# Optimization experiments

Measured on AMD Instinct MI355X. Metric: run time of the kernel, lower is better.

The kernel has to match this reference:

```python
import jax, jax.numpy as jnp
import numpy as np

LAMBDA_TV = 0.01
RHO = 1.0
MAX_ITER = 10
CG_ITER = 10


def _fft2c(x):
    # x: (B, 2, H, W) real/imag stacked -> centered ortho FFT, same layout
    xc = x[:, 0] + 1j * x[:, 1]
    kc = jnp.fft.fftshift(
        jnp.fft.fft2(jnp.fft.ifftshift(xc, axes=(-2, -1)), norm='ortho'),
        axes=(-2, -1))
    return jnp.stack([kc.real, kc.imag], axis=1)


def _ifft2c(x):
    xc = x[:, 0] + 1j * x[:, 1]
    ic = jnp.fft.fftshift(
        jnp.fft.ifft2(jnp.fft.ifftshift(xc, axes=(-2, -1)), norm='ortho'),
        axes=(-2, -1))
    return jnp.stack([ic.real, ic.imag], axis=1)


def _gradient(x):
    # forward differences, zero at the far boundary; cat along channel dim
    dx = jnp.concatenate([x[..., 1:] - x[..., :-1], jnp.zeros_like(x[..., :1])], axis=-1)
    dy = jnp.concatenate([x[..., 1:, :] - x[..., :-1, :], jnp.zeros_like(x[..., :1, :])], axis=-2)
    return jnp.concatenate([dx, dy], axis=1)


def _divergence(p):
    # Faithful to the original: only uses channels 0 and 1 of p -> (B,1,H,W)
    px, py = p[:, 0:1], p[:, 1:2]
    div_x = jnp.concatenate(
        [px[..., 0:1], px[..., 1:-1] - px[..., :-2], -px[..., -2:-1]], axis=-1)
    div_y = jnp.concatenate(
        [py[..., 0:1, :], py[..., 1:-1, :] - py[..., :-2, :], -py[..., -2:-1, :]], axis=-2)
    return div_x + div_y


def soft_threshold(x, t):
    return jnp.sign(x) * jnp.maximum(jnp.abs(x) - t, 0.0)


def _cg_solve(x0, b, mask):
    # Solves (F^H M F + rho * D^H D) x = b with early-stop semantics of the original
    def A(z):
        return _ifft2c(mask * _fft2c(z)) - RHO * _divergence(_gradient(z))

    r0 = b - A(x0)
    rsold0 = jnp.sum(r0 * r0)

    def step(carry, _):
        x, r, p, rsold, done = carry
        Ap = A(p)
        alpha = rsold / (jnp.sum(p * Ap) + 1e-12)
        xn = x + alpha * p
        rn = r - alpha * Ap
        rsnew = jnp.sum(rn * rn)
        stop = rsnew < 1e-10
        pn = rn + (rsnew / rsold) * p
        x = jnp.where(done, x, xn)
        r = jnp.where(done, r, rn)
        p = jnp.where(done | stop, p, pn)
        rsold = jnp.where(done | stop, rsold, rsnew)
        done = done | stop
        return (x, r, p, rsold, done), None

    init = (x0, r0, r0, rsold0, jnp.array(False))
    (x, _, _, _, _), _ = jax.lax.scan(step, init, None, length=CG_ITER)
    return x


def reference(y, mask):
    x0 = _ifft2c(y)
    u0 = _gradient(x0)
    v0 = jnp.zeros_like(u0)
    b_data = _ifft2c(mask * y)  # constant across outer iterations
    thresh = LAMBDA_TV / RHO

    def step(carry, _):
        x, u, v, done, count, pres_l, dres_l = carry
        b = b_data + RHO * _divergence(u - v)
        xn = _cg_solve(x, b, mask)
        g = _gradient(xn)
        un = soft_threshold(g + v, thresh)
        vn = v + g - un
        pres = jnp.linalg.norm(g - un)
        dres = jnp.linalg.norm(RHO * _divergence(un - u))
        stop = (pres < 1e-4) & (dres < 1e-4)
        x = jnp.where(done, x, xn)
        u = jnp.where(done, u, un)
        v = jnp.where(done, v, vn)
        pres_l = jnp.where(done, pres_l, pres)
        dres_l = jnp.where(done, dres_l, dres)
        count = count + (1 - done.astype(jnp.int32))
        done = done | stop
        return (x, u, v, done, count, pres_l, dres_l), None

    init = (x0, u0, v0, jnp.array(False), jnp.array(0, jnp.int32),
            jnp.array(0.0, x0.dtype), jnp.array(0.0, x0.dtype))
    (x, _, _, _, count, pres, dres), _ = jax.lax.scan(step, init, None, length=MAX_ITER)
    return x, count, pres, dres


def setup_inputs() -> dict:
    key = jax.random.key(0)
    k1, k2 = jax.random.split(key)
    B, H, W = 4, 320, 320
    y = jax.random.normal(k1, (B, 2, H, W), dtype=jnp.float32)
    mask = (jax.random.uniform(k2, (B, 1, H, W)) < 0.3).astype(jnp.float32)
    return {"y": y, "mask": mask}
```

## Files before the change

### kernel.cpp

```cpp
#include <hip/hip_runtime.h>
#include <math.h>

#define DEVFN __device__ __forceinline__

namespace {

constexpr int NW = 320, NH = 320, NHW = NW * NH, NB = 4;
constexpr int NC2 = 2 * NHW;
constexpr int GRID = NB * NH;
constexpr int NTHR = 320;
constexpr float THRESHc = 0.01f;

struct C2 { float x, y; };
DEVFN C2 cmul(C2 a, C2 b) { return C2{a.x * b.x - a.y * b.y, a.x * b.y + a.y * b.x}; }

template <int SIGN>
DEVFN C2 TW(const float2* tw, int m) {
  float2 t = tw[m];
  return C2{t.x, (SIGN < 0) ? t.y : -t.y};
}

DEVFN int swzcol(int bid) { return (bid & 7) * (GRID / 8) + (bid >> 3); }

DEVFN int oidx(int t) { return 5 * (t & 63) + (t >> 6); }

DEVFN void wavebar() {
  __builtin_amdgcn_wave_barrier();
  asm volatile("" ::: "memory");
}

template <int SIGN, bool MASKED>
__device__ C2 fftp_core(const float2* IN, float2* SCR, const float2* tw, int t,
                        const float* __restrict__ misRow) {
  const int q = t >> 6, n1 = t & 63;
  float2* lo = SCR + q * 128;
  float2* hi = lo + 64;
  float mval = 1.f;
  if (MASKED) mval = misRow[5 * n1 + q];
  C2 acc;
  {
    float2 v0 = IN[n1];
    acc.x = v0.x; acc.y = v0.y;
#pragma unroll
    for (int n2 = 1; n2 < 5; n2++) {
      float2 v = IN[n1 + 64 * n2];
      C2 w = TW<SIGN>(tw, 64 * ((n2 * q) % 5));
      acc.x += v.x * w.x - v.y * w.y;
      acc.y += v.x * w.y + v.y * w.x;
    }
    acc = cmul(acc, TW<SIGN>(tw, n1 * q));
  }
  lo[n1] = make_float2(acc.x, acc.y);
  wavebar();
  {
    C2 s{0.f, 0.f};
    int rr = n1 & 3, base = n1 >> 2;
#pragma unroll
    for (int p = 0; p < 4; p++) {
      float2 v = lo[base + 16 * p];
      C2 w = TW<SIGN>(tw, 80 * ((p * rr) & 3));
      s.x += v.x * w.x - v.y * w.y;
      s.y += v.x * w.y + v.y * w.x;
    }
    hi[n1] = make_float2(s.x, s.y);
  }
  wavebar();
  {
    C2 s{0.f, 0.f};
    int rr = n1 & 15, base = ((n1 >> 4) << 2) + (n1 & 3);
#pragma unroll
    for (int p = 0; p < 4; p++) {
      float2 v = hi[base + 16 * p];
      C2 w = TW<SIGN>(tw, 20 * ((p * rr) & 15));
      s.x += v.x * w.x - v.y * w.y;
      s.y += v.x * w.y + v.y * w.x;
    }
    lo[n1] = make_float2(s.x, s.y);
  }
  wavebar();
  {
    C2 s{0.f, 0.f};
    int base = n1 & 15;
#pragma unroll
    for (int p = 0; p < 4; p++) {
      float2 v = lo[base + 16 * p];
      C2 w = TW<SIGN>(tw, 5 * ((p * n1) & 63));
      s.x += v.x * w.x - v.y * w.y;
      s.y += v.x * w.y + v.y * w.x;
    }
    acc = s;
  }
  if (MASKED) { acc.x *= mval; acc.y *= mval; }
  return acc;
}

DEVFN float Gfunc2(const float2* __restrict__ z, int b, int h, int w) {
  const float2* zz = z + b * NHW;
  int hw = h * NW + w;
  float divx, divy;
  if (w == 0) {
    divx = zz[hw + 1].x - zz[hw].x;
  } else if (w < NW - 1) {
    divx = (zz[hw + 1].x - zz[hw].x) - (zz[hw].x - zz[hw - 1].x);
  } else {
    divx = -(zz[hw].x - zz[hw - 1].x);
  }
  if (h == 0) {
    divy = (w < NW - 1) ? zz[hw + 1].y - zz[hw].y : 0.f;
  } else if (h < NH - 1) {
    float a = (w < NW - 1) ? zz[hw + 1].y - zz[hw].y : 0.f;
    float bb = (w < NW - 1) ? zz[hw - NW + 1].y - zz[hw - NW].y : 0.f;
    divy = a - bb;
  } else {
    divy = -((w < NW - 1) ? zz[hw - NW + 1].y - zz[hw - NW].y : 0.f);
  }
  return divx + divy;
}

DEVFN float divUV(const float* __restrict__ u, const float* __restrict__ v, int b, int h, int w) {
  const float* u0 = u + (b * 4 + 0) * NHW; const float* v0 = v + (b * 4 + 0) * NHW;
  const float* u1 = u + (b * 4 + 1) * NHW; const float* v1 = v + (b * 4 + 1) * NHW;
  int hw = h * NW + w;
  float divx, divy;
  if (w == 0)          divx = u0[hw] - v0[hw];
  else if (w < NW - 1) divx = (u0[hw] - v0[hw]) - (u0[hw - 1] - v0[hw - 1]);
  else                 divx = -(u0[hw - 1] - v0[hw - 1]);
  if (h == 0)          divy = u1[hw] - v1[hw];
  else if (h < NH - 1) divy = (u1[hw] - v1[hw]) - (u1[hw - NW] - v1[hw - NW]);
  else                 divy = -(u1[hw - NW] - v1[hw - NW]);
  return divx + divy;
}

DEVFN double shflxd(double v, int m) {
  union { double d; int i[2]; } a; a.d = v;
  a.i[0] = __shfl_xor(a.i[0], m, 64);
  a.i[1] = __shfl_xor(a.i[1], m, 64);
  return a.d;
}
DEVFN double waveRed(double v) {
#pragma unroll
  for (int m = 32; m; m >>= 1) v += shflxd(v, m);
  return v;
}

__device__ double redParts(const double* __restrict__ part, double* sdot, int t) {
  double v = part[t] + part[t + 320] + part[t + 640] + part[t + 960];
  v = waveRed(v);
  if ((t & 63) == 0) sdot[t >> 6] = v;
  __syncthreads();
  double s = sdot[0] + sdot[1] + sdot[2] + sdot[3] + sdot[4];
  __syncthreads();
  return s;
}

__device__ void blockDot1(double a, double* sdot, int t, double* outp) {
  a = waveRed(a);
  if ((t & 63) == 0) sdot[t >> 6] = a;
  __syncthreads();
  if (t == 0) *outp = sdot[0] + sdot[1] + sdot[2] + sdot[3] + sdot[4];
  __syncthreads();
}

__device__ void blockDot3(double a, double b, double c, double* sdot, int t,
                          double* o0, double* o1, double* o2, int bid) {
  a = waveRed(a); b = waveRed(b); c = waveRed(c);
  int wv = t >> 6;
  if ((t & 63) == 0) { sdot[wv * 3] = a; sdot[wv * 3 + 1] = b; sdot[wv * 3 + 2] = c; }
  __syncthreads();
  if (t == 0) {
    double s0 = 0, s1 = 0, s2 = 0;
#pragma unroll
    for (int w2 = 0; w2 < 5; w2++) { s0 += sdot[w2 * 3]; s1 += sdot[w2 * 3 + 1]; s2 += sdot[w2 * 3 + 2]; }
    o0[bid] = s0; o1[bid] = s1; o2[bid] = s2;
  }
  __syncthreads();
}

#define FFTK_SHARED                                     \
  __shared__ float2 sA[320];                            \
  __shared__ float2 sB[320];                            \
  __shared__ float2 sS[640];                            \
  __shared__ float2 stw[320];                           \
  __shared__ double sdot[16];                           \
  (void)sdot;                                           \
  const int t = threadIdx.x;                            \
  const int bid = blockIdx.x;                           \
  stw[t] = twg[t];



__global__ __launch_bounds__(NTHR) void k_init(const float* __restrict__ mask,
                                               float* __restrict__ misT, float2* __restrict__ tw) {
  int t = threadIdx.x, bid = blockIdx.x;
  if (bid == 0) {
    double ang = -2.0 * 3.14159265358979323846 * (double)t / 320.0;
    tw[t] = make_float2((float)cos(ang), (float)sin(ang));
  }
  int i = bid * NTHR + t;
  int b = i / NHW, hw = i % NHW, h = hw / NW, w = hw % NW;
  int hs = (h + 160) % 320, ws = (w + 160) % 320;
  misT[b * NHW + w * NW + h] = mask[b * NHW + hs * NW + ws] * (1.0f / 102400.0f);
}

__global__ __launch_bounds__(NTHR) void k0a(const float* __restrict__ y, const float* __restrict__ mask,
                                            float2* __restrict__ tA, float2* __restrict__ tB,
                                            const float2* __restrict__ twg) {
  FFTK_SHARED
  const int wid = swzcol(bid);
  const int gb = wid / NH, gl = wid % NH;
  const int rowBase = gb * NC2 + gl * NW;
  float sgn = (t & 1) ? -1.f : 1.f;
  sA[t] = make_float2(sgn * y[rowBase + t], sgn * y[rowBase + NHW + t]);
  __syncthreads();
  C2 a1 = fftp_core<1, false>(sA, sS, stw, t, nullptr);
  const int o = oidx(t);
  const float sgo = (o & 1) ? -1.f : 1.f;
  tA[gb * NHW + o * NW + gl] = make_float2(sgo * a1.x, sgo * a1.y);
  __syncthreads();
  float m = mask[gb * NHW + gl * NW + t];
  sA[t] = make_float2(sgn * m * y[rowBase + t], sgn * m * y[rowBase + NHW + t]);
  __syncthreads();
  C2 a2 = fftp_core<1, false>(sA, sS, stw, t, nullptr);
  tB[gb * NHW + o * NW + gl] = make_float2(sgo * a2.x, sgo * a2.y);
}

__global__ __launch_bounds__(NTHR) void k0b(const float2* __restrict__ tA, const float2* __restrict__ tB,
                                            float2* __restrict__ x2, float2* __restrict__ bdata2,
                                            const float2* __restrict__ twg) {
  FFTK_SHARED
  const int wid = swzcol(bid);
  const int gb = wid / NH, gl = wid % NH;
  float sgn = (t & 1) ? -1.f : 1.f;
  {
    float2 v = tA[gb * NHW + gl * NW + t];
    sA[t] = make_float2(sgn * v.x, sgn * v.y);
  }
  __syncthreads();
  C2 a1 = fftp_core<1, false>(sA, sS, stw, t, nullptr);
  const int o = oidx(t);
  const float so = ((o & 1) ? -1.f : 1.f) * (1.f / 320.f);
  x2[gb * NHW + o * NW + gl] = make_float2(a1.x * so, a1.y * so);
  __syncthreads();
  {
    float2 v = tB[gb * NHW + gl * NW + t];
    sA[t] = make_float2(sgn * v.x, sgn * v.y);
  }
  __syncthreads();
  C2 a2 = fftp_core<1, false>(sA, sS, stw, t, nullptr);
  bdata2[gb * NHW + o * NW + gl] = make_float2(a2.x * so, a2.y * so);
}

__global__ __launch_bounds__(NTHR) void ka0(const float2* __restrict__ x2, float2* __restrict__ xc2,
                                            float* __restrict__ u, float* __restrict__ v,
                                            float2* __restrict__ tA, const float2* __restrict__ twg) {
  FFTK_SHARED
  const int wid = swzcol(bid);
  const int gb = wid / NH, gl = wid % NH;
  {
    int i = bid * NTHR + t;
    int b = i / NHW, hw = i % NHW, h = hw / NW, w = hw % NW;
    const float2* zz = x2 + b * NHW;
    float2 z0 = zz[hw];
    float g0 = 0, g1 = 0, g2 = 0, g3 = 0;
    if (w < NW - 1) { float2 zr = zz[hw + 1]; g0 = zr.x - z0.x; g1 = zr.y - z0.y; }
    if (h < NH - 1) { float2 zd = zz[hw + NW]; g2 = zd.x - z0.x; g3 = zd.y - z0.y; }
    int b4 = b * 4 * NHW;
    u[b4 + hw] = g0;           v[b4 + hw] = 0.f;
    u[b4 + NHW + hw] = g1;     v[b4 + NHW + hw] = 0.f;
    u[b4 + 2 * NHW + hw] = g2; v[b4 + 2 * NHW + hw] = 0.f;
    u[b4 + 3 * NHW + hw] = g3; v[b4 + 3 * NHW + hw] = 0.f;
  }
  int idx = gb * NHW + gl * NW + t;
  float2 xv = x2[idx];
  xc2[idx] = xv;
  sA[t] = xv;
  __syncthreads();
  C2 a = fftp_core<-1, false>(sA, sS, stw, t, nullptr);
  tA[gb * NHW + oidx(t) * NW + gl] = make_float2(a.x, a.y);
}

__global__ __launch_bounds__(NTHR) void kb(const float2* __restrict__ tA, float2* __restrict__ tB,
                                           const float* __restrict__ misT,
                                           const float* __restrict__ un, const float* __restrict__ vn,
                                           float* __restrict__ u, float* __restrict__ v,
                                           const double* __restrict__ pPaPrev, const double* __restrict__ pPbPrev,
                                           double* __restrict__ hist_pres, double* __restrict__ hist_dres,
                                           const float2* __restrict__ twg, int it) {
  FFTK_SHARED
  const int wid = swzcol(bid);
  const int gb = wid / NH, gl = wid % NH;
  if (it > 0) {
    double ppa = redParts(pPaPrev, sdot, t);
    double ppb = redParts(pPbPrev, sdot, t);
    if (bid == 0 && t == 0) { hist_pres[it - 1] = ppa; hist_dres[it - 1] = ppb; }
    bool doneA = false;
    for (int j = 0; j <= it - 2; j++) {
      float pr = sqrtf((float)hist_pres[j]), dr = sqrtf((float)hist_dres[j]);
      doneA |= (pr < 1e-4f && dr < 1e-4f);
    }
    if (!doneA) {
      for (int i = wid * NTHR + t; i < NB * 4 * NHW; i += GRID * NTHR) { u[i] = un[i]; v[i] = vn[i]; }
    }
  }
  sA[t] = tA[gb * NHW + gl * NW + t];
  __syncthreads();
  C2 a1 = fftp_core<-1, true>(sA, sS, stw, t, misT + gb * NHW + gl * NW);
  const int o = oidx(t);
  sB[o] = make_float2(a1.x, a1.y);
  __syncthreads();
  C2 a2 = fftp_core<1, false>(sB, sS, stw, t, nullptr);
  tB[gb * NHW + o * NW + gl] = make_float2(a2.x, a2.y);
}

__global__ __launch_bounds__(NTHR) void kcd(const float2* __restrict__ tB, float2* __restrict__ tA,
                                            const float2* __restrict__ x2,
                                            const float* __restrict__ u, const float* __restrict__ v,
                                            const float2* __restrict__ bdata2, float2* __restrict__ r2,
                                            float2* __restrict__ p2, double* __restrict__ pRS,
                                            const float2* __restrict__ twg) {
  FFTK_SHARED
  const int wid = swzcol(bid);
  const int gb = wid / NH, gl = wid % NH;
  sA[t] = tB[gb * NHW + gl * NW + t];
  __syncthreads();
  C2 a1 = fftp_core<1, false>(sA, sS, stw, t, nullptr);
  const int o = oidx(t);
  const int idxO = gb * NHW + gl * NW + o;
  float G = Gfunc2(x2, gb, gl, o);
  float d = divUV(u, v, gb, gl, o);
  float2 bd = bdata2[idxO];
  float rr = (bd.x + d) - (a1.x - G);
  float ri = (bd.y + d) - (a1.y - G);
  float2 rv = make_float2(rr, ri);
  r2[idxO] = rv; p2[idxO] = rv;
  double acc = (double)rr * rr + (double)ri * ri;
  blockDot1(acc, sdot, t, &pRS[bid]);
  sA[o] = rv;
  __syncthreads();
  C2 a2 = fftp_core<-1, false>(sA, sS, stw, t, nullptr);
  tA[gb * NHW + o * NW + gl] = make_float2(a2.x, a2.y);
}

__global__ __launch_bounds__(NTHR) void kd(float2* __restrict__ xc2, float2* __restrict__ r2,
                                           float2* __restrict__ p2, const float2* __restrict__ Ap2,
                                           float2* __restrict__ tA, const double* __restrict__ pRS,
                                           const double* __restrict__ pD0, const double* __restrict__ pD1,
                                           const double* __restrict__ pD2, double* __restrict__ hist_rs,
                                           const float2* __restrict__ twg, int k) {
  FFTK_SHARED
  const int wid = swzcol(bid);
  const int gb = wid / NH, gl = wid % NH;
  const int idx = gb * NHW + gl * NW + t;
  double pAp = redParts(pD0, sdot, t);
  double rAp = redParts(pD1, sdot, t);
  double A2  = redParts(pD2, sdot, t);
  double rsold = (k == 1) ? redParts(pRS, sdot, t) : hist_rs[k - 2];
  float alpha = (float)rsold / ((float)pAp + 1e-12f);
  double rsnew = rsold - 2.0 * (double)alpha * rAp + (double)alpha * (double)alpha * A2;
  if (bid == 0 && t == 0) hist_rs[k - 1] = rsnew;
  bool doneIn = false;
  for (int j = 0; j <= k - 2; j++) doneIn |= ((float)hist_rs[j] < 1e-10f);
  bool stop = ((float)rsnew < 1e-10f);
  bool doneP = doneIn || stop;
  float beta = (float)rsnew / (float)rsold;
  float2 pv = p2[idx], rv = r2[idx], av = Ap2[idx], xv = xc2[idx];
  if (!doneIn) {
    xv.x += alpha * pv.x; xv.y += alpha * pv.y;
    rv.x -= alpha * av.x; rv.y -= alpha * av.y;
  }
  float2 pn = doneP ? pv : make_float2(rv.x + beta * pv.x, rv.y + beta * pv.y);
  xc2[idx] = xv; r2[idx] = rv; p2[idx] = pn;
  sA[t] = pn;
  __syncthreads();
  C2 a = fftp_core<-1, false>(sA, sS, stw, t, nullptr);
  tA[gb * NHW + oidx(t) * NW + gl] = make_float2(a.x, a.y);
}

__global__ __launch_bounds__(NTHR) void ke(const float2* __restrict__ tA, float2* __restrict__ tB,
                                           const float* __restrict__ misT,
                                           const float2* __restrict__ twg) {
  FFTK_SHARED
  const int wid = swzcol(bid);
  const int gb = wid / NH, gl = wid % NH;
  sA[t] = tA[gb * NHW + gl * NW + t];
  __syncthreads();
  C2 a1 = fftp_core<-1, true>(sA, sS, stw, t, misT + gb * NHW + gl * NW);
  const int o = oidx(t);
  sB[o] = make_float2(a1.x, a1.y);
  __syncthreads();
  C2 a2 = fftp_core<1, false>(sB, sS, stw, t, nullptr);
  tB[gb * NHW + o * NW + gl] = make_float2(a2.x, a2.y);
}

__global__ __launch_bounds__(NTHR) void kf(const float2* __restrict__ tB, const float2* __restrict__ p2,
                                           const float2* __restrict__ r2, float2* __restrict__ Ap2,
                                           double* __restrict__ pD0, double* __restrict__ pD1,
                                           double* __restrict__ pD2, const float2* __restrict__ twg) {
  FFTK_SHARED
  const int wid = swzcol(bid);
  const int gb = wid / NH, gl = wid % NH;
  sA[t] = tB[gb * NHW + gl * NW + t];
  __syncthreads();
  C2 a = fftp_core<1, false>(sA, sS, stw, t, nullptr);
  const int o = oidx(t);
  const int idxO = gb * NHW + gl * NW + o;
  float G = Gfunc2(p2, gb, gl, o);
  float Ar = a.x - G, Ai = a.y - G;
  Ap2[idxO] = make_float2(Ar, Ai);
  float2 pv = p2[idxO], rv = r2[idxO];
  double aP = (double)pv.x * Ar + (double)pv.y * Ai;
  double aR = (double)rv.x * Ar + (double)rv.y * Ai;
  double aA = (double)Ar * Ar + (double)Ai * Ai;
  blockDot3(aP, aR, aA, sdot, t, pD0, pD1, pD2, bid);
}

__global__ __launch_bounds__(NTHR) void kh1(const float2* __restrict__ xc2, const float2* __restrict__ p2,
                                            const float* __restrict__ v, float2* __restrict__ tB,
                                            float* __restrict__ un, float* __restrict__ vn,
                                            const double* __restrict__ pD0, const double* __restrict__ hist_rs,
                                            double* __restrict__ pPaCur) {
  __shared__ double sdot[16];
  const int t = threadIdx.x, bid = blockIdx.x;
  double pAp = redParts(pD0, sdot, t);
  double rsold = hist_rs[8];
  float alphaF = (float)rsold / ((float)pAp + 1e-12f);
  bool doneX = false;
  for (int j = 0; j <= 8; j++) doneX |= ((float)hist_rs[j] < 1e-10f);
  int i = bid * NTHR + t;
  int b = i / NHW, hw = i % NHW, h = hw / NW, w = hw % NW;
  int base2 = b * NHW;
  auto XN = [&](int off) {
    float2 vv = xc2[base2 + off];
    if (!doneX) {
      float2 pp = p2[base2 + off];
      vv.x += alphaF * pp.x; vv.y += alphaF * pp.y;
    }
    return vv;
  };
  float2 x0 = XN(hw);
  float g0 = 0, g1 = 0, g2 = 0, g3 = 0;
  if (w < NW - 1) { float2 xr = XN(hw + 1); g0 = xr.x - x0.x; g1 = xr.y - x0.y; }
  if (h < NH - 1) { float2 xd = XN(hw + NW); g2 = xd.x - x0.x; g3 = xd.y - x0.y; }
  tB[base2 + hw] = x0;
  float gs[4] = {g0, g1, g2, g3};
  double acc = 0.0;
#pragma unroll
  for (int ch = 0; ch < 4; ch++) {
    int ui = (b * 4 + ch) * NHW + hw;
    float vv = v[ui];
    float sv = gs[ch] + vv;
    float a2 = fabsf(sv) - THRESHc;
    float uo = (a2 > 0.f) ? copysignf(a2, sv) : 0.f;
    un[ui] = uo;
    vn[ui] = vv + gs[ch] - uo;
    float dd = gs[ch] - uo;
    acc += (double)dd * dd;
  }
  blockDot1(acc, sdot, t, &pPaCur[bid]);
}

__global__ __launch_bounds__(NTHR) void kh2a(float2* __restrict__ x2, float2* __restrict__ xc2,
                                             const float2* __restrict__ tB, float2* __restrict__ tA,
                                             const float* __restrict__ un,
                                             const float* __restrict__ u,
                                             const double* __restrict__ hist_pres,
                                             const double* __restrict__ hist_dres,
                                             double* __restrict__ pPbCur,
                                             const float2* __restrict__ twg, int it) {
  FFTK_SHARED
  const int wid = swzcol(bid);
  const int gb = wid / NH, gl = wid % NH;
  const int idx = gb * NHW + gl * NW + t;
  bool doneA = false;
  for (int j = 0; j <= it - 1; j++) {
    float pr = sqrtf((float)hist_pres[j]), dr = sqrtf((float)hist_dres[j]);
    doneA |= (pr < 1e-4f && dr < 1e-4f);
  }
  {
    int i = bid * NTHR + t;
    int b = i / NHW, hw = i % NHW, h = hw / NW, w = hw % NW;
    const float* N0 = un + (b * 4 + 0) * NHW; const float* U0 = u + (b * 4 + 0) * NHW;
    const float* N1 = un + (b * 4 + 1) * NHW; const float* U1 = u + (b * 4 + 1) * NHW;
    float divx, divy;
    if (w == 0)          divx = N0[hw] - U0[hw];
    else if (w < NW - 1) divx = (N0[hw] - U0[hw]) - (N0[hw - 1] - U0[hw - 1]);
    else                 divx = -(N0[hw - 1] - U0[hw - 1]);
    if (h == 0)          divy = N1[hw] - U1[hw];
    else if (h < NH - 1) divy = (N1[hw] - U1[hw]) - (N1[hw - NW] - U1[hw - NW]);
    else                 divy = -(N1[hw - NW] - U1[hw - NW]);
    float d = divx + divy;
    double acc = (double)d * d;
    blockDot1(acc, sdot, t, &pPbCur[bid]);
  }
  float2 xn = tB[idx];
  float2 xf = doneA ? x2[idx] : xn;
  x2[idx] = xf; xc2[idx] = xf;
  sA[t] = xf;
  __syncthreads();
  C2 a = fftp_core<-1, false>(sA, sS, stw, t, nullptr);
  tA[gb * NHW + oidx(t) * NW + gl] = make_float2(a.x, a.y);
}

__global__ __launch_bounds__(NTHR) void k_out(const float2* __restrict__ x2,
                                              const double* __restrict__ hist_pres,
                                              const double* __restrict__ hist_dres,
                                              const double* __restrict__ pPa9,
                                              const double* __restrict__ pPb9,
                                              float* __restrict__ out) {
  __shared__ double sdot[16];
  const int t = threadIdx.x, bid = blockIdx.x;
  {
    int i = bid * NTHR + t;
    int b = i / NHW, hw = i % NHW;
    float2 v = x2[b * NHW + hw];
    out[b * NC2 + hw] = v.x;
    out[b * NC2 + NHW + hw] = v.y;
  }
  if (bid == 0) {
    double p9 = redParts(pPa9, sdot, t);
    double d9 = redParts(pPb9, sdot, t);
    if (t == 0) {
      int count = 0; bool done = false; float presO = 0.f, dresO = 0.f;
      for (int it = 0; it < 10; ++it) {
        double hp = (it == 9) ? p9 : hist_pres[it];
        double hd = (it == 9) ? d9 : hist_dres[it];
        if (!done) {
          count++;
          presO = sqrtf((float)hp);
          dresO = sqrtf((float)hd);
          done = (presO < 1e-4f) && (dresO < 1e-4f);
        }
      }
      out[NB * NC2 + 0] = (float)count;
      out[NB * NC2 + 1] = presO;
      out[NB * NC2 + 2] = dresO;
    }
  }
}

}

extern "C" void kernel_launch(void* const* d_in, const int* in_sizes, int n_in,
                              void* d_out, int out_size, void* d_ws, size_t ws_size,
                              hipStream_t stream) {
  (void)in_sizes; (void)n_in; (void)out_size; (void)ws_size;
  const float* y = (const float*)d_in[0];
  const float* mask = (const float*)d_in[1];
  float* out = (float*)d_out;
  float* wsf = (float*)d_ws;

  double* dws = (double*)wsf;
  double* pRS       = dws;
  double* pD0       = dws + 1280;
  double* pD1       = dws + 2560;
  double* pD2       = dws + 3840;
  double* pPa       = dws + 5120;
  double* pPb       = dws + 7680;
  double* hist_rs   = dws + 10240;
  double* hist_pres = dws + 10256;
  double* hist_dres = dws + 10272;

  float* fb = wsf + 20576;
  float2* tw = (float2*)fb; fb += 640;
  float* misT = fb; fb += (size_t)NB * NHW;
  float2* tA = (float2*)fb; fb += (size_t)2 * NB * NHW;
  float2* tB = (float2*)fb; fb += (size_t)2 * NB * NHW;
  auto take2 = [&](size_t n) { float2* ptr = (float2*)fb; fb += 2 * n; return ptr; };
  float2* x2     = take2((size_t)NB * NHW);
  float2* xc2    = take2((size_t)NB * NHW);
  float2* r2     = take2((size_t)NB * NHW);
  float2* p2     = take2((size_t)NB * NHW);
  float2* Ap2    = take2((size_t)NB * NHW);
  float2* bdata2 = take2((size_t)NB * NHW);
  auto take = [&](size_t n) { float* ptr = fb; fb += n; return ptr; };
  float* u  = take((size_t)NB * 4 * NHW);
  float* v  = take((size_t)NB * 4 * NHW);
  float* un = take((size_t)NB * 4 * NHW);
  float* vn = take((size_t)NB * 4 * NHW);

  k_init<<<GRID, NTHR, 0, stream>>>(mask, misT, tw);
  k0a<<<GRID, NTHR, 0, stream>>>(y, mask, tA, tB, tw);
  k0b<<<GRID, NTHR, 0, stream>>>(tA, tB, x2, bdata2, tw);
  ka0<<<GRID, NTHR, 0, stream>>>(x2, xc2, u, v, tA, tw);

  for (int it = 0; it < 10; ++it) {
    int prevPar = (it + 1) & 1;
    int curPar = it & 1;
    kb<<<GRID, NTHR, 0, stream>>>(tA, tB, misT, un, vn, u, v,
                                  pPa + prevPar * 1280, pPb + prevPar * 1280,
                                  hist_pres, hist_dres, tw, it);
    kcd<<<GRID, NTHR, 0, stream>>>(tB, tA, x2, u, v, bdata2, r2, p2, pRS, tw);
    ke<<<GRID, NTHR, 0, stream>>>(tA, tB, misT, tw);
    kf<<<GRID, NTHR, 0, stream>>>(tB, p2, r2, Ap2, pD0, pD1, pD2, tw);
    for (int k = 1; k < 10; ++k) {
      kd<<<GRID, NTHR, 0, stream>>>(xc2, r2, p2, Ap2, tA, pRS, pD0, pD1, pD2, hist_rs, tw, k);
      ke<<<GRID, NTHR, 0, stream>>>(tA, tB, misT, tw);
      kf<<<GRID, NTHR, 0, stream>>>(tB, p2, r2, Ap2, pD0, pD1, pD2, tw);
    }
    kh1<<<GRID, NTHR, 0, stream>>>(xc2, p2, v, tB, un, vn, pD0, hist_rs, pPa + curPar * 1280);
    kh2a<<<GRID, NTHR, 0, stream>>>(x2, xc2, tB, tA, un, u, hist_pres, hist_dres,
                                    pPb + curPar * 1280, tw, it);
  }
  k_out<<<GRID, NTHR, 0, stream>>>(x2, hist_pres, hist_dres, pPa + 1280, pPb + 1280, out);
}
```

Baseline: 2.741 ms.

## Restructure CG to run in row-FFT domain, merging kernels per CG step

Rewrites the CG inner loop so the vectors (x, r, p, Ap) are kept in the row-transformed domain. Each CG step becomes two launches instead of three. The first launch runs a 2x grid: half the blocks update vectors and produce the spatial p, the other half apply the masked column FFT pair. The second launch does the gradient-divergence term plus the dot products. The precomputed transposed mask table is dropped in favour of reading the mask directly with a shifted index, and r/p are ping-ponged across two buffers. This cuts the kernel count and one transposed global pass per CG step, but adds an extra FFT for the gradient term and more complex buffer parity logic.

```diff
diff --git a/kernel.cpp b/kernel.cpp
--- a/kernel.cpp
+++ b/kernel.cpp
@@ -31,12 +31,16 @@
 
 template <int SIGN, bool MASKED>
 __device__ C2 fftp_core(const float2* IN, float2* SCR, const float2* tw, int t,
-                        const float* __restrict__ misRow) {
+                        const float* __restrict__ maskCol) {
   const int q = t >> 6, n1 = t & 63;
   float2* lo = SCR + q * 128;
   float2* hi = lo + 64;
   float mval = 1.f;
-  if (MASKED) mval = misRow[5 * n1 + q];
+  if (MASKED) {
+    int ks = 5 * n1 + q + 160;
+    if (ks >= 320) ks -= 320;
+    mval = maskCol[ks * NW] * 0.003125f;
+  }
   C2 acc;
   {
     float2 v0 = IN[n1];
@@ -182,28 +186,21 @@
   __shared__ float2 sS[640];                            \
   __shared__ float2 stw[320];                           \
   __shared__ double sdot[16];                           \
-  (void)sdot;                                           \
+  (void)sdot; (void)sB;                                 \
   const int t = threadIdx.x;                            \
   const int bid = blockIdx.x;                           \
   stw[t] = twg[t];
 
 
 
-__global__ __launch_bounds__(NTHR) void k_init(const float* __restrict__ mask,
-                                               float* __restrict__ misT, float2* __restrict__ tw) {
-  int t = threadIdx.x, bid = blockIdx.x;
-  if (bid == 0) {
-    double ang = -2.0 * 3.14159265358979323846 * (double)t / 320.0;
-    tw[t] = make_float2((float)cos(ang), (float)sin(ang));
-  }
-  int i = bid * NTHR + t;
-  int b = i / NHW, hw = i % NHW, h = hw / NW, w = hw % NW;
-  int hs = (h + 160) % 320, ws = (w + 160) % 320;
-  misT[b * NHW + w * NW + h] = mask[b * NHW + hs * NW + ws] * (1.0f / 102400.0f);
+__global__ __launch_bounds__(NTHR) void k_init(float2* __restrict__ tw) {
+  int t = threadIdx.x;
+  double ang = -2.0 * 3.14159265358979323846 * (double)t / 320.0;
+  tw[t] = make_float2((float)cos(ang), (float)sin(ang));
 }
 
 __global__ __launch_bounds__(NTHR) void k0a(const float* __restrict__ y, const float* __restrict__ mask,
-                                            float2* __restrict__ tA, float2* __restrict__ tB,
+                                            float2* __restrict__ s1, float2* __restrict__ s2,
                                             const float2* __restrict__ twg) {
   FFTK_SHARED
   const int wid = swzcol(bid);
@@ -215,16 +212,16 @@
   C2 a1 = fftp_core<1, false>(sA, sS, stw, t, nullptr);
   const int o = oidx(t);
   const float sgo = (o & 1) ? -1.f : 1.f;
-  tA[gb * NHW + o * NW + gl] = make_float2(sgo * a1.x, sgo * a1.y);
+  s1[gb * NHW + o * NW + gl] = make_float2(sgo * a1.x, sgo * a1.y);
   __syncthreads();
   float m = mask[gb * NHW + gl * NW + t];
   sA[t] = make_float2(sgn * m * y[rowBase + t], sgn * m * y[rowBase + NHW + t]);
   __syncthreads();
   C2 a2 = fftp_core<1, false>(sA, sS, stw, t, nullptr);
-  tB[gb * NHW + o * NW + gl] = make_float2(sgo * a2.x, sgo * a2.y);
-}
-
-__global__ __launch_bounds__(NTHR) void k0b(const float2* __restrict__ tA, const float2* __restrict__ tB,
+  s2[gb * NHW + o * NW + gl] = make_float2(sgo * a2.x, sgo * a2.y);
+}
+
+__global__ __launch_bounds__(NTHR) void k0b(const float2* __restrict__ s1, const float2* __restrict__ s2,
                                             float2* __restrict__ x2, float2* __restrict__ bdata2,
                                             const float2* __restrict__ twg) {
   FFTK_SHARED
@@ -232,7 +229,7 @@
   const int gb = wid / NH, gl = wid % NH;
   float sgn = (t & 1) ? -1.f : 1.f;
   {
-    float2 v = tA[gb * NHW + gl * NW + t];
+    float2 v = s1[gb * NHW + gl * NW + t];
     sA[t] = make_float2(sgn * v.x, sgn * v.y);
   }
   __syncthreads();
@@ -242,7 +239,7 @@
   x2[gb * NHW + o * NW + gl] = make_float2(a1.x * so, a1.y * so);
   __syncthreads();
   {
-    float2 v = tB[gb * NHW + gl * NW + t];
+    float2 v = s2[gb * NHW + gl * NW + t];
     sA[t] = make_float2(sgn * v.x, sgn * v.y);
   }
   __syncthreads();
@@ -250,9 +247,9 @@
   bdata2[gb * NHW + o * NW + gl] = make_float2(a2.x * so, a2.y * so);
 }
 
-__global__ __launch_bounds__(NTHR) void ka0(const float2* __restrict__ x2, float2* __restrict__ xc2,
+__global__ __launch_bounds__(NTHR) void ka0(const float2* __restrict__ x2,
                                             float* __restrict__ u, float* __restrict__ v,
-                                            float2* __restrict__ tA, const float2* __restrict__ twg) {
+                                            float2* __restrict__ xrow, const float2* __restrict__ twg) {
   FFTK_SHARED
   const int wid = swzcol(bid);
   const int gb = wid / NH, gl = wid % NH;
@@ -270,17 +267,14 @@
     u[b4 + 2 * NHW + hw] = g2; v[b4 + 2 * NHW + hw] = 0.f;
     u[b4 + 3 * NHW + hw] = g3; v[b4 + 3 * NHW + hw] = 0.f;
   }
-  int idx = gb * NHW + gl * NW + t;
-  float2 xv = x2[idx];
-  xc2[idx] = xv;
-  sA[t] = xv;
+  sA[t] = x2[gb * NHW + gl * NW + t];
   __syncthreads();
   C2 a = fftp_core<-1, false>(sA, sS, stw, t, nullptr);
-  tA[gb * NHW + oidx(t) * NW + gl] = make_float2(a.x, a.y);
-}
-
-__global__ __launch_bounds__(NTHR) void kb(const float2* __restrict__ tA, float2* __restrict__ tB,
-                                           const float* __restrict__ misT,
+  xrow[gb * NHW + gl * NW + oidx(t)] = make_float2(a.x, a.y);
+}
+
+__global__ __launch_bounds__(NTHR) void kb(const float2* __restrict__ xrow, float2* __restrict__ Mt,
+                                           const float* __restrict__ mask,
                                            const float* __restrict__ un, const float* __restrict__ vn,
                                            float* __restrict__ u, float* __restrict__ v,
                                            const double* __restrict__ pPaPrev, const double* __restrict__ pPbPrev,
@@ -302,146 +296,177 @@
       for (int i = wid * NTHR + t; i < NB * 4 * NHW; i += GRID * NTHR) { u[i] = un[i]; v[i] = vn[i]; }
     }
   }
-  sA[t] = tA[gb * NHW + gl * NW + t];
-  __syncthreads();
-  C2 a1 = fftp_core<-1, true>(sA, sS, stw, t, misT + gb * NHW + gl * NW);
+  sA[t] = xrow[gb * NHW + t * NW + gl];
+  __syncthreads();
+  C2 a1 = fftp_core<-1, true>(sA, sS, stw, t, mask + gb * NHW + ((gl + 160) % 320));
   const int o = oidx(t);
   sB[o] = make_float2(a1.x, a1.y);
   __syncthreads();
   C2 a2 = fftp_core<1, false>(sB, sS, stw, t, nullptr);
-  tB[gb * NHW + o * NW + gl] = make_float2(a2.x, a2.y);
-}
-
-__global__ __launch_bounds__(NTHR) void kcd(const float2* __restrict__ tB, float2* __restrict__ tA,
-                                            const float2* __restrict__ x2,
+  Mt[gb * NHW + o * NW + gl] = make_float2(a2.x, a2.y);
+}
+
+__global__ __launch_bounds__(NTHR) void kcd(const float2* __restrict__ Mt, const float2* __restrict__ x2,
                                             const float* __restrict__ u, const float* __restrict__ v,
-                                            const float2* __restrict__ bdata2, float2* __restrict__ r2,
-                                            float2* __restrict__ p2, double* __restrict__ pRS,
-                                            const float2* __restrict__ twg) {
-  FFTK_SHARED
-  const int wid = swzcol(bid);
-  const int gb = wid / NH, gl = wid % NH;
-  sA[t] = tB[gb * NHW + gl * NW + t];
-  __syncthreads();
-  C2 a1 = fftp_core<1, false>(sA, sS, stw, t, nullptr);
+                                            const float2* __restrict__ bdata2,
+                                            float2* __restrict__ rOut, float2* __restrict__ pOut,
+                                            double* __restrict__ pRS, const float2* __restrict__ twg) {
+  FFTK_SHARED
+  const int wid = swzcol(bid);
+  const int gb = wid / NH, gl = wid % NH;
+  const int base = gb * NHW + gl * NW;
+  {
+    float d = divUV(u, v, gb, gl, t);
+    float2 bd = bdata2[base + t];
+    sA[t] = make_float2(bd.x + d, bd.y + d);
+  }
+  __syncthreads();
+  C2 bt = fftp_core<-1, false>(sA, sS, stw, t, nullptr);
+  __syncthreads();
+  {
+    float Gx = Gfunc2(x2, gb, gl, t);
+    sA[t] = make_float2(Gx, Gx);
+  }
+  __syncthreads();
+  C2 gt = fftp_core<-1, false>(sA, sS, stw, t, nullptr);
   const int o = oidx(t);
-  const int idxO = gb * NHW + gl * NW + o;
-  float G = Gfunc2(x2, gb, gl, o);
-  float d = divUV(u, v, gb, gl, o);
-  float2 bd = bdata2[idxO];
-  float rr = (bd.x + d) - (a1.x - G);
-  float ri = (bd.y + d) - (a1.y - G);
-  float2 rv = make_float2(rr, ri);
-  r2[idxO] = rv; p2[idxO] = rv;
-  double acc = (double)rr * rr + (double)ri * ri;
+  float2 mx = Mt[base + o];
+  float rr = bt.x - mx.x + gt.x;
+  float ri = bt.y - mx.y + gt.y;
+  rOut[base + o] = make_float2(rr, ri);
+  pOut[base + o] = make_float2(rr, ri);
+  double acc = ((double)rr * rr + (double)ri * ri) * (1.0 / 320.0);
   blockDot1(acc, sdot, t, &pRS[bid]);
-  sA[o] = rv;
-  __syncthreads();
-  C2 a2 = fftp_core<-1, false>(sA, sS, stw, t, nullptr);
-  tA[gb * NHW + o * NW + gl] = make_float2(a2.x, a2.y);
-}
-
-__global__ __launch_bounds__(NTHR) void kd(float2* __restrict__ xc2, float2* __restrict__ r2,
-                                           float2* __restrict__ p2, const float2* __restrict__ Ap2,
-                                           float2* __restrict__ tA, const double* __restrict__ pRS,
-                                           const double* __restrict__ pD0, const double* __restrict__ pD1,
-                                           const double* __restrict__ pD2, double* __restrict__ hist_rs,
-                                           const float2* __restrict__ twg, int k) {
-  FFTK_SHARED
-  const int wid = swzcol(bid);
-  const int gb = wid / NH, gl = wid % NH;
-  const int idx = gb * NHW + gl * NW + t;
-  double pAp = redParts(pD0, sdot, t);
-  double rAp = redParts(pD1, sdot, t);
-  double A2  = redParts(pD2, sdot, t);
-  double rsold = (k == 1) ? redParts(pRS, sdot, t) : hist_rs[k - 2];
-  float alpha = (float)rsold / ((float)pAp + 1e-12f);
-  double rsnew = rsold - 2.0 * (double)alpha * rAp + (double)alpha * (double)alpha * A2;
-  if (bid == 0 && t == 0) hist_rs[k - 1] = rsnew;
-  bool doneIn = false;
-  for (int j = 0; j <= k - 2; j++) doneIn |= ((float)hist_rs[j] < 1e-10f);
-  bool stop = ((float)rsnew < 1e-10f);
-  bool doneP = doneIn || stop;
-  float beta = (float)rsnew / (float)rsold;
-  float2 pv = p2[idx], rv = r2[idx], av = Ap2[idx], xv = xc2[idx];
-  if (!doneIn) {
-    xv.x += alpha * pv.x; xv.y += alpha * pv.y;
-    rv.x -= alpha * av.x; rv.y -= alpha * av.y;
-  }
-  float2 pn = doneP ? pv : make_float2(rv.x + beta * pv.x, rv.y + beta * pv.y);
-  xc2[idx] = xv; r2[idx] = rv; p2[idx] = pn;
-  sA[t] = pn;
-  __syncthreads();
-  C2 a = fftp_core<-1, false>(sA, sS, stw, t, nullptr);
-  tA[gb * NHW + oidx(t) * NW + gl] = make_float2(a.x, a.y);
-}
-
-__global__ __launch_bounds__(NTHR) void ke(const float2* __restrict__ tA, float2* __restrict__ tB,
-                                           const float* __restrict__ misT,
+}
+
+__global__ __launch_bounds__(NTHR) void kD1(float2* __restrict__ xrow,
+                                            const float2* __restrict__ rIn, float2* __restrict__ rOut,
+                                            const float2* __restrict__ pIn, float2* __restrict__ pOut,
+                                            const float2* __restrict__ Aprow,
+                                            float2* __restrict__ psp, float2* __restrict__ Mt,
+                                            const float* __restrict__ mask,
+                                            const double* __restrict__ pRS,
+                                            const double* __restrict__ pD0, const double* __restrict__ pD1a,
+                                            const double* __restrict__ pD2a, double* __restrict__ hist_rs,
+                                            const float2* __restrict__ twg, int k) {
+  FFTK_SHARED
+  const bool isCol = (bid >= GRID);
+  const int sb = isCol ? bid - GRID : bid;
+  const int wid = swzcol(sb);
+  const int gb = wid / NH, gl = wid % NH;
+  float alpha = 0.f, beta = 0.f;
+  bool doneIn = false, doneP = false;
+  if (k >= 1) {
+    double pAp = redParts(pD0, sdot, t);
+    double rAp = redParts(pD1a, sdot, t);
+    double A2  = redParts(pD2a, sdot, t);
+    double rsold = (k == 1) ? redParts(pRS, sdot, t) : hist_rs[k - 2];
+    alpha = (float)rsold / ((float)pAp + 1e-12f);
+    double rsnew = rsold - 2.0 * (double)alpha * rAp + (double)alpha * (double)alpha * A2;
+    if (bid == 0 && t == 0) hist_rs[k - 1] = rsnew;
+    for (int j = 0; j <= k - 2; j++) doneIn |= ((float)hist_rs[j] < 1e-10f);
+    bool stop = ((float)rsnew < 1e-10f);
+    doneP = doneIn || stop;
+    beta = (float)rsnew / (float)rsold;
+  }
+  if (!isCol) {
+    const int base = gb * NHW + gl * NW;
+    float2 pv = pIn[base + t];
+    if (k >= 1) {
+      float2 rv = rIn[base + t], av = Aprow[base + t], xv = xrow[base + t];
+      if (!doneIn) {
+        xv.x += alpha * pv.x; xv.y += alpha * pv.y;
+        rv.x -= alpha * av.x; rv.y -= alpha * av.y;
+      }
+      float2 pn = doneP ? pv : make_float2(rv.x + beta * pv.x, rv.y + beta * pv.y);
+      xrow[base + t] = xv; rOut[base + t] = rv; pOut[base + t] = pn;
+      pv = pn;
+    }
+    sA[t] = pv;
+    __syncthreads();
+    C2 a = fftp_core<1, false>(sA, sS, stw, t, nullptr);
+    psp[base + oidx(t)] = make_float2(a.x * (1.f / 320.f), a.y * (1.f / 320.f));
+  } else {
+    const int cidx = gb * NHW + t * NW + gl;
+    float2 pv = pIn[cidx];
+    if (k >= 1) {
+      float2 rv = rIn[cidx], av = Aprow[cidx];
+      if (!doneIn) { rv.x -= alpha * av.x; rv.y -= alpha * av.y; }
+      if (!doneP) { pv.x = rv.x + beta * pv.x; pv.y = rv.y + beta * pv.y; }
+    }
+    sA[t] = pv;
+    __syncthreads();
+    C2 a1 = fftp_core<-1, true>(sA, sS, stw, t, mask + gb * NHW + ((gl + 160) % 320));
+    const int o = oidx(t);
+    sB[o] = make_float2(a1.x, a1.y);
+    __syncthreads();
+    C2 a2 = fftp_core<1, false>(sB, sS, stw, t, nullptr);
+    Mt[gb * NHW + o * NW + gl] = make_float2(a2.x, a2.y);
+  }
+}
+
+__global__ __launch_bounds__(NTHR) void kD2(const float2* __restrict__ Mt, const float2* __restrict__ psp,
+                                            const float2* __restrict__ pCur, const float2* __restrict__ rCur,
+                                            float2* __restrict__ Aprow,
+                                            double* __restrict__ pD0, double* __restrict__ pD1a,
+                                            double* __restrict__ pD2a, const float2* __restrict__ twg) {
+  FFTK_SHARED
+  const int wid = swzcol(bid);
+  const int gb = wid / NH, gl = wid % NH;
+  const int base = gb * NHW + gl * NW;
+  {
+    float Gv = Gfunc2(psp, gb, gl, t);
+    sA[t] = make_float2(Gv, Gv);
+  }
+  __syncthreads();
+  C2 g = fftp_core<-1, false>(sA, sS, stw, t, nullptr);
+  const int o = oidx(t);
+  float2 mv = Mt[base + o];
+  float Ar = mv.x - g.x, Ai = mv.y - g.y;
+  Aprow[base + o] = make_float2(Ar, Ai);
+  float2 pv = pCur[base + o], rv = rCur[base + o];
+  double aP = ((double)pv.x * Ar + (double)pv.y * Ai) * (1.0 / 320.0);
+  double aR = ((double)rv.x * Ar + (double)rv.y * Ai) * (1.0 / 320.0);
+  double aA = ((double)Ar * Ar + (double)Ai * Ai) * (1.0 / 320.0);
+  blockDot3(aP, aR, aA, sdot, t, pD0, pD1a, pD2a, bid);
+}
+
+__global__ __launch_bounds__(NTHR) void kX(const float2* __restrict__ xrow, const float2* __restrict__ pCur,
+                                           float2* __restrict__ psp,
+                                           const double* __restrict__ pD0, const double* __restrict__ hist_rs,
                                            const float2* __restrict__ twg) {
   FFTK_SHARED
   const int wid = swzcol(bid);
   const int gb = wid / NH, gl = wid % NH;
-  sA[t] = tA[gb * NHW + gl * NW + t];
-  __syncthreads();
-  C2 a1 = fftp_core<-1, true>(sA, sS, stw, t, misT + gb * NHW + gl * NW);
-  const int o = oidx(t);
-  sB[o] = make_float2(a1.x, a1.y);
-  __syncthreads();
-  C2 a2 = fftp_core<1, false>(sB, sS, stw, t, nullptr);
-  tB[gb * NHW + o * NW + gl] = make_float2(a2.x, a2.y);
-}
-
-__global__ __launch_bounds__(NTHR) void kf(const float2* __restrict__ tB, const float2* __restrict__ p2,
-                                           const float2* __restrict__ r2, float2* __restrict__ Ap2,
-                                           double* __restrict__ pD0, double* __restrict__ pD1,
-                                           double* __restrict__ pD2, const float2* __restrict__ twg) {
-  FFTK_SHARED
-  const int wid = swzcol(bid);
-  const int gb = wid / NH, gl = wid % NH;
-  sA[t] = tB[gb * NHW + gl * NW + t];
-  __syncthreads();
-  C2 a = fftp_core<1, false>(sA, sS, stw, t, nullptr);
-  const int o = oidx(t);
-  const int idxO = gb * NHW + gl * NW + o;
-  float G = Gfunc2(p2, gb, gl, o);
-  float Ar = a.x - G, Ai = a.y - G;
-  Ap2[idxO] = make_float2(Ar, Ai);
-  float2 pv = p2[idxO], rv = r2[idxO];
-  double aP = (double)pv.x * Ar + (double)pv.y * Ai;
-  double aR = (double)rv.x * Ar + (double)rv.y * Ai;
-  double aA = (double)Ar * Ar + (double)Ai * Ai;
-  blockDot3(aP, aR, aA, sdot, t, pD0, pD1, pD2, bid);
-}
-
-__global__ __launch_bounds__(NTHR) void kh1(const float2* __restrict__ xc2, const float2* __restrict__ p2,
-                                            const float* __restrict__ v, float2* __restrict__ tB,
-                                            float* __restrict__ un, float* __restrict__ vn,
-                                            const double* __restrict__ pD0, const double* __restrict__ hist_rs,
-                                            double* __restrict__ pPaCur) {
-  __shared__ double sdot[16];
-  const int t = threadIdx.x, bid = blockIdx.x;
   double pAp = redParts(pD0, sdot, t);
   double rsold = hist_rs[8];
   float alphaF = (float)rsold / ((float)pAp + 1e-12f);
   bool doneX = false;
   for (int j = 0; j <= 8; j++) doneX |= ((float)hist_rs[j] < 1e-10f);
+  const int base = gb * NHW + gl * NW;
+  float2 xv = xrow[base + t];
+  if (!doneX) {
+    float2 pp = pCur[base + t];
+    xv.x += alphaF * pp.x; xv.y += alphaF * pp.y;
+  }
+  sA[t] = xv;
+  __syncthreads();
+  C2 a = fftp_core<1, false>(sA, sS, stw, t, nullptr);
+  psp[base + oidx(t)] = make_float2(a.x * (1.f / 320.f), a.y * (1.f / 320.f));
+}
+
+__global__ __launch_bounds__(NTHR) void kh1p(const float2* __restrict__ xn, const float* __restrict__ v,
+                                             float* __restrict__ un, float* __restrict__ vn,
+                                             double* __restrict__ pPaCur) {
+  __shared__ double sdot[16];
+  const int t = threadIdx.x, bid = blockIdx.x;
   int i = bid * NTHR + t;
   int b = i / NHW, hw = i % NHW, h = hw / NW, w = hw % NW;
-  int base2 = b * NHW;
-  auto XN = [&](int off) {
-    float2 vv = xc2[base2 + off];
-    if (!doneX) {
-      float2 pp = p2[base2 + off];
-      vv.x += alphaF * pp.x; vv.y += alphaF * pp.y;
-    }
-    return vv;
-  };
-  float2 x0 = XN(hw);
+  const float2* zz = xn + b * NHW;
+  float2 x0 = zz[hw];
   float g0 = 0, g1 = 0, g2 = 0, g3 = 0;
-  if (w < NW - 1) { float2 xr = XN(hw + 1); g0 = xr.x - x0.x; g1 = xr.y - x0.y; }
-  if (h < NH - 1) { float2 xd = XN(hw + NW); g2 = xd.x - x0.x; g3 = xd.y - x0.y; }
-  tB[base2 + hw] = x0;
+  if (w < NW - 1) { float2 xr = zz[hw + 1]; g0 = xr.x - x0.x; g1 = xr.y - x0.y; }
+  if (h < NH - 1) { float2 xd = zz[hw + NW]; g2 = xd.x - x0.x; g3 = xd.y - x0.y; }
   float gs[4] = {g0, g1, g2, g3};
   double acc = 0.0;
 #pragma unroll
@@ -459,10 +484,9 @@
   blockDot1(acc, sdot, t, &pPaCur[bid]);
 }
 
-__global__ __launch_bounds__(NTHR) void kh2a(float2* __restrict__ x2, float2* __restrict__ xc2,
-                                             const float2* __restrict__ tB, float2* __restrict__ tA,
-                                             const float* __restrict__ un,
-                                             const float* __restrict__ u,
+__global__ __launch_bounds__(NTHR) void kh2a(float2* __restrict__ x2, const float2* __restrict__ psp,
+                                             float2* __restrict__ xrow,
+                                             const float* __restrict__ un, const float* __restrict__ u,
                                              const double* __restrict__ hist_pres,
                                              const double* __restrict__ hist_dres,
                                              double* __restrict__ pPbCur,
@@ -492,13 +516,13 @@
     double acc = (double)d * d;
     blockDot1(acc, sdot, t, &pPbCur[bid]);
   }
-  float2 xn = tB[idx];
-  float2 xf = doneA ? x2[idx] : xn;
-  x2[idx] = xf; xc2[idx] = xf;
+  float2 xnv = psp[idx];
+  float2 xf = doneA ? x2[idx] : xnv;
+  x2[idx] = xf;
   sA[t] = xf;
   __syncthreads();
   C2 a = fftp_core<-1, false>(sA, sS, stw, t, nullptr);
-  tA[gb * NHW + oidx(t) * NW + gl] = make_float2(a.x, a.y);
+  xrow[gb * NHW + gl * NW + oidx(t)] = make_float2(a.x, a.y);
 }
 
 __global__ __launch_bounds__(NTHR) void k_out(const float2* __restrict__ x2,
@@ -552,8 +576,8 @@
   double* dws = (double*)wsf;
   double* pRS       = dws;
   double* pD0       = dws + 1280;
-  double* pD1       = dws + 2560;
-  double* pD2       = dws + 3840;
+  double* pD1a      = dws + 2560;
+  double* pD2a      = dws + 3840;
   double* pPa       = dws + 5120;
   double* pPb       = dws + 7680;
   double* hist_rs   = dws + 10240;
@@ -562,15 +586,16 @@
 
   float* fb = wsf + 20576;
   float2* tw = (float2*)fb; fb += 640;
-  float* misT = fb; fb += (size_t)NB * NHW;
-  float2* tA = (float2*)fb; fb += (size_t)2 * NB * NHW;
-  float2* tB = (float2*)fb; fb += (size_t)2 * NB * NHW;
   auto take2 = [&](size_t n) { float2* ptr = (float2*)fb; fb += 2 * n; return ptr; };
+  float2* xrow   = take2((size_t)NB * NHW);
+  float2* rr0    = take2((size_t)NB * NHW);
+  float2* rr1    = take2((size_t)NB * NHW);
+  float2* pr0    = take2((size_t)NB * NHW);
+  float2* pr1    = take2((size_t)NB * NHW);
+  float2* Aprow  = take2((size_t)NB * NHW);
+  float2* Mt     = take2((size_t)NB * NHW);
+  float2* psp    = take2((size_t)NB * NHW);
   float2* x2     = take2((size_t)NB * NHW);
-  float2* xc2    = take2((size_t)NB * NHW);
-  float2* r2     = take2((size_t)NB * NHW);
-  float2* p2     = take2((size_t)NB * NHW);
-  float2* Ap2    = take2((size_t)NB * NHW);
   float2* bdata2 = take2((size_t)NB * NHW);
   auto take = [&](size_t n) { float* ptr = fb; fb += n; return ptr; };
   float* u  = take((size_t)NB * 4 * NHW);
@@ -578,27 +603,34 @@
   float* un = take((size_t)NB * 4 * NHW);
   float* vn = take((size_t)NB * 4 * NHW);
 
-  k_init<<<GRID, NTHR, 0, stream>>>(mask, misT, tw);
-  k0a<<<GRID, NTHR, 0, stream>>>(y, mask, tA, tB, tw);
-  k0b<<<GRID, NTHR, 0, stream>>>(tA, tB, x2, bdata2, tw);
-  ka0<<<GRID, NTHR, 0, stream>>>(x2, xc2, u, v, tA, tw);
+  float2* RR[2] = {rr0, rr1};
+  float2* PR[2] = {pr0, pr1};
+
+  k_init<<<1, NTHR, 0, stream>>>(tw);
+  k0a<<<GRID, NTHR, 0, stream>>>(y, mask, Mt, Aprow, tw);
+  k0b<<<GRID, NTHR, 0, stream>>>(Mt, Aprow, x2, bdata2, tw);
+  ka0<<<GRID, NTHR, 0, stream>>>(x2, u, v, xrow, tw);
 
   for (int it = 0; it < 10; ++it) {
     int prevPar = (it + 1) & 1;
     int curPar = it & 1;
-    kb<<<GRID, NTHR, 0, stream>>>(tA, tB, misT, un, vn, u, v,
+    kb<<<GRID, NTHR, 0, stream>>>(xrow, Mt, mask, un, vn, u, v,
                                   pPa + prevPar * 1280, pPb + prevPar * 1280,
                                   hist_pres, hist_dres, tw, it);
-    kcd<<<GRID, NTHR, 0, stream>>>(tB, tA, x2, u, v, bdata2, r2, p2, pRS, tw);
-    ke<<<GRID, NTHR, 0, stream>>>(tA, tB, misT, tw);
-    kf<<<GRID, NTHR, 0, stream>>>(tB, p2, r2, Ap2, pD0, pD1, pD2, tw);
-    for (int k = 1; k < 10; ++k) {
-      kd<<<GRID, NTHR, 0, stream>>>(xc2, r2, p2, Ap2, tA, pRS, pD0, pD1, pD2, hist_rs, tw, k);
-      ke<<<GRID, NTHR, 0, stream>>>(tA, tB, misT, tw);
-      kf<<<GRID, NTHR, 0, stream>>>(tB, p2, r2, Ap2, pD0, pD1, pD2, tw);
-    }
-    kh1<<<GRID, NTHR, 0, stream>>>(xc2, p2, v, tB, un, vn, pD0, hist_rs, pPa + curPar * 1280);
-    kh2a<<<GRID, NTHR, 0, stream>>>(x2, xc2, tB, tA, un, u, hist_pres, hist_dres,
+    kcd<<<GRID, NTHR, 0, stream>>>(Mt, x2, u, v, bdata2, RR[1], PR[1], pRS, tw);
+    for (int k = 0; k < 10; ++k) {
+      int in = (k == 0) ? 1 : (k & 1);
+      int outp = in ^ 1;
+      kD1<<<2 * GRID, NTHR, 0, stream>>>(xrow, RR[in], RR[outp], PR[in], PR[outp],
+                                         Aprow, psp, Mt, mask,
+                                         pRS, pD0, pD1a, pD2a, hist_rs, tw, k);
+      int cur = (k == 0) ? 1 : outp;
+      kD2<<<GRID, NTHR, 0, stream>>>(Mt, psp, PR[cur], RR[cur], Aprow,
+                                     pD0, pD1a, pD2a, tw);
+    }
+    kX<<<GRID, NTHR, 0, stream>>>(xrow, PR[0], psp, pD0, hist_rs, tw);
+    kh1p<<<GRID, NTHR, 0, stream>>>(psp, v, un, vn, pPa + curPar * 1280);
+    kh2a<<<GRID, NTHR, 0, stream>>>(x2, psp, xrow, un, u, hist_pres, hist_dres,
                                     pPb + curPar * 1280, tw, it);
   }
   k_out<<<GRID, NTHR, 0, stream>>>(x2, hist_pres, hist_dres, pPa + 1280, pPb + 1280, out);
```

Result: slower. 3.259 ms (+18.9%).
